# Kernel tuning notes

Hardware: AMD Instinct MI355X
Metric: run time of the kernel (lower is better)

## Reference

```python
import jax, jax.numpy as jnp
import numpy as np

B, C, H, W = 4, 128, 64, 64
CQK = C // 8


def setup_inputs() -> dict:
    key = jax.random.key(0)
    ks = jax.random.split(key, 8)
    s = 0.02
    return {
        "x": jax.random.normal(ks[0], (B, C, H, W), dtype=jnp.float32),
        "Wq": jax.random.normal(ks[1], (CQK, C), dtype=jnp.float32) * s,
        "bq": jnp.zeros((CQK,), dtype=jnp.float32),
        "Wk": jax.random.normal(ks[2], (CQK, C), dtype=jnp.float32) * s,
        "bk": jnp.zeros((CQK,), dtype=jnp.float32),
        "Wv": jax.random.normal(ks[3], (C, C), dtype=jnp.float32) * s,
        "bv": jnp.zeros((C,), dtype=jnp.float32),
        "gamma": jnp.zeros((1,), dtype=jnp.float32),
    }


def reference(x, Wq, bq, Wk, bk, Wv, bv, gamma):
    b, c, h, w = x.shape
    xf = x.reshape(b, c, h * w)                      # [b, c, n]
    # 1x1 convs == per-position channel matmuls
    q = jnp.einsum('dc,bcn->bdn', Wq, xf) + bq[None, :, None]   # [b, c/8, n]
    k = jnp.einsum('dc,bcn->bdn', Wk, xf) + bk[None, :, None]   # [b, c/8, n]
    v = jnp.einsum('ec,bcn->ben', Wv, xf) + bv[None, :, None]   # [b, c, n]
    energy = jnp.einsum('bdi,bdj->bij', q, k)        # [b, n, n]
    attn = jax.nn.softmax(energy, axis=-1)           # softmax over keys j
    out = jnp.einsum('bcj,bij->bci', v, attn)        # [b, c, n]
    out = out.reshape(b, c, h, w)
    return gamma[0] * out + x
```

## Files before the change

kernel.cpp:

```cpp
#include <hip/hip_runtime.h>
#include <hip/hip_bf16.h>


#define BN 4
#define CC 128
#define NN 4096
#define DQK 16
#define KVB 64

typedef float f32x16 __attribute__((ext_vector_type(16)));
typedef short s16x8 __attribute__((ext_vector_type(8)));
typedef unsigned short u16;

union FragU { unsigned u[4]; s16x8 v; };

__device__ inline u16 to_bf16(float f) {
  __hip_bfloat16 h = __float2bfloat16(f);
  return *reinterpret_cast<u16*>(&h);
}
__device__ inline unsigned pack_bf16(float lo, float hi) {
  return ((unsigned)to_bf16(hi) << 16) | (unsigned)to_bf16(lo);
}
__device__ inline float bf16lo_f(unsigned u) {
  return __builtin_bit_cast(float, u << 16);
}
__device__ inline float bf16hi_f(unsigned u) {
  return __builtin_bit_cast(float, u & 0xffff0000u);
}

__global__ __launch_bounds__(320) void proj_kernel(
    const float* __restrict__ x,
    const float* __restrict__ Wq, const float* __restrict__ bq,
    const float* __restrict__ Wk, const float* __restrict__ bk,
    const float* __restrict__ Wv, const float* __restrict__ bv,
    u16* __restrict__ Qt, u16* __restrict__ Kt, u16* __restrict__ Vb)
{
  __shared__ float xs[CC * 32];
  const int tid = threadIdx.x;
  const int wave = tid >> 6;
  const int lane = tid & 63;
  const int l31 = lane & 31, h = lane >> 5;
  const int bid = blockIdx.x;
  const int b = bid >> 7;
  const int n0 = (bid & 127) * 32;

  const float* xb = x + ((size_t)b * CC) * NN + n0;
  #pragma unroll
  for (int k = 0; k < 4; ++k) {
    int idx4 = tid + 320 * k;
    if (idx4 < 1024) {
      int c = idx4 >> 3;
      int nn4 = (idx4 & 7) * 4;
      float4 vv = *reinterpret_cast<const float4*>(xb + (size_t)c * NN + nn4);
      *reinterpret_cast<float4*>(&xs[c * 32 + nn4]) = vv;
    }
  }
  __syncthreads();

  s16x8 bx[8];
  #pragma unroll
  for (int ks = 0; ks < 8; ++ks) {
    FragU f;
    #pragma unroll
    for (int q = 0; q < 4; ++q) {
      int c = 16 * ks + 8 * h + 2 * q;
      f.u[q] = pack_bf16(xs[c * 32 + l31], xs[(c + 1) * 32 + l31]);
    }
    bx[ks] = f.v;
  }

  f32x16 acc;
  #pragma unroll
  for (int r = 0; r < 16; ++r) acc[r] = 0.f;

  const float LOG2E = 1.44269504088896340736f;

  if (wave == 0) {
    const float* wrow = (l31 < 16) ? (Wq + (size_t)l31 * CC)
                                   : (Wk + (size_t)(l31 - 16) * CC);
    #pragma unroll
    for (int ks = 0; ks < 8; ++ks) {
      const float* wp = wrow + 16 * ks + 8 * h;
      float4 w0 = *reinterpret_cast<const float4*>(wp);
      float4 w1 = *reinterpret_cast<const float4*>(wp + 4);
      FragU a;
      a.u[0] = pack_bf16(w0.x, w0.y); a.u[1] = pack_bf16(w0.z, w0.w);
      a.u[2] = pack_bf16(w1.x, w1.y); a.u[3] = pack_bf16(w1.z, w1.w);
      acc = __builtin_amdgcn_mfma_f32_32x32x16_bf16(a.v, bx[ks], acc, 0, 0, 0);
    }
    #pragma unroll
    for (int r = 0; r < 16; ++r) {
      int row = (r & 3) + 8 * (r >> 2) + 4 * h;
      float val = acc[r];
      if (row < 16) {
        val = (val + bq[row]) * LOG2E;
        Qt[((size_t)b * NN + n0 + l31) * DQK + row] = to_bf16(val);
      } else {
        val += bk[row - 16];
        Kt[((size_t)b * NN + n0 + l31) * DQK + (row - 16)] = to_bf16(val);
      }
    }
  } else {
    const int rt = wave - 1;
    const float* vrow = Wv + (size_t)(rt * 32 + l31) * CC;
    #pragma unroll
    for (int ks = 0; ks < 8; ++ks) {
      const float* wp = vrow + 16 * ks + 8 * h;
      float4 w0 = *reinterpret_cast<const float4*>(wp);
      float4 w1 = *reinterpret_cast<const float4*>(wp + 4);
      FragU a;
      a.u[0] = pack_bf16(w0.x, w0.y); a.u[1] = pack_bf16(w0.z, w0.w);
      a.u[2] = pack_bf16(w1.x, w1.y); a.u[3] = pack_bf16(w1.z, w1.w);
      acc = __builtin_amdgcn_mfma_f32_32x32x16_bf16(a.v, bx[ks], acc, 0, 0, 0);
    }
    #pragma unroll
    for (int r = 0; r < 16; ++r) {
      int e = rt * 32 + (r & 3) + 8 * (r >> 2) + 4 * h;
      Vb[((size_t)b * CC + e) * NN + n0 + l31] = to_bf16(acc[r] + bv[e]);
    }
  }
}

__global__ __launch_bounds__(512, 4) void flash_kernel(
    const u16* __restrict__ Qt, const u16* __restrict__ Kt,
    const u16* __restrict__ Vb,
    u16* __restrict__ Opart, float* __restrict__ mstat,
    float* __restrict__ lstat, int JS)
{
  __shared__ u16 Vs[2][CC * KVB];
  const int tid = threadIdx.x;
  const int wv = tid >> 6;
  const int lane = tid & 63;
  const int l31 = lane & 31, h = lane >> 5;
  const int qb = blockIdx.x & 15;
  const int bs = blockIdx.x >> 4;
  const int b = bs / JS, sg = bs % JS;
  const int i0 = qb * 256 + wv * 32;
  const int seglen = NN / JS;
  const int j_begin = sg * seglen;
  const int niter = seglen / KVB;

  const int sc0 = tid >> 3;
  const int so = (tid & 7) * 16;
  const int sw0 = (sc0 & 7) << 4;

  const u16* Kb = Kt + (size_t)b * NN * DQK;
  const u16* Vbb = Vb + (size_t)b * CC * NN;

  s16x8 qf = *reinterpret_cast<const s16x8*>(
      Qt + ((size_t)b * NN + i0 + l31) * DQK + 8 * h);

  f32x16 zero;
  #pragma unroll
  for (int r = 0; r < 16; ++r) zero[r] = 0.f;
  f32x16 acc[4];
  #pragma unroll
  for (int ct = 0; ct < 4; ++ct) acc[ct] = zero;
  float m_run = -__builtin_inff();
  float l_run = 0.f;

  {
    s16x8 g0 = *reinterpret_cast<const s16x8*>(
        Vbb + (size_t)sc0 * NN + j_begin + so / 2);
    s16x8 g1 = *reinterpret_cast<const s16x8*>(
        Vbb + (size_t)(64 + sc0) * NN + j_begin + so / 2);
    *reinterpret_cast<s16x8*>(&Vs[0][sc0 * KVB + ((so ^ sw0) >> 1)]) = g0;
    *reinterpret_cast<s16x8*>(&Vs[0][(64 + sc0) * KVB + ((so ^ sw0) >> 1)]) = g1;
  }
  s16x8 kf0 = *reinterpret_cast<const s16x8*>(
      Kb + (size_t)(j_begin + l31) * DQK + 8 * h);
  s16x8 kf1 = *reinterpret_cast<const s16x8*>(
      Kb + (size_t)(j_begin + 32 + l31) * DQK + 8 * h);
  __syncthreads();

  const int rsw = (l31 & 7) << 4;

  for (int t = 0; t < niter; ++t) {
    const int cur = t & 1;
    s16x8 g0, g1, nk0, nk1;
    const bool more = (t + 1 < niter);
    if (more) {
      const int jn = j_begin + (t + 1) * KVB;
      g0 = *reinterpret_cast<const s16x8*>(
          Vbb + (size_t)sc0 * NN + jn + so / 2);
      g1 = *reinterpret_cast<const s16x8*>(
          Vbb + (size_t)(64 + sc0) * NN + jn + so / 2);
      nk0 = *reinterpret_cast<const s16x8*>(
          Kb + (size_t)(jn + l31) * DQK + 8 * h);
      nk1 = *reinterpret_cast<const s16x8*>(
          Kb + (size_t)(jn + 32 + l31) * DQK + 8 * h);
    }

    #pragma unroll
    for (int s = 0; s < 2; ++s) {
      f32x16 sv = __builtin_amdgcn_mfma_f32_32x32x16_bf16(
          s ? kf1 : kf0, qf, zero, 0, 0, 0);

      float mx01 = fmaxf(sv[0], sv[1]),  mx23 = fmaxf(sv[2], sv[3]);
      float mx45 = fmaxf(sv[4], sv[5]),  mx67 = fmaxf(sv[6], sv[7]);
      float mx89 = fmaxf(sv[8], sv[9]),  mxab = fmaxf(sv[10], sv[11]);
      float mxcd = fmaxf(sv[12], sv[13]), mxef = fmaxf(sv[14], sv[15]);
      float tmax = fmaxf(fmaxf(fmaxf(mx01, mx23), fmaxf(mx45, mx67)),
                         fmaxf(fmaxf(mx89, mxab), fmaxf(mxcd, mxef)));
      float cmb = fmaxf(tmax, __shfl_xor(tmax, 32));
      float m_new = (cmb > m_run + 8.f) ? cmb : m_run;
      if (__any(m_new > m_run)) {
        float alpha = __builtin_amdgcn_exp2f(m_run - m_new);
        l_run *= alpha;
        #pragma unroll
        for (int ct = 0; ct < 4; ++ct)
          #pragma unroll
          for (int r = 0; r < 16; ++r) acc[ct][r] *= alpha;
        m_run = m_new;
      }

      float p[16];
      #pragma unroll
      for (int r = 0; r < 16; ++r)
        p[r] = __builtin_amdgcn_exp2f(sv[r] - m_run);
      float s01 = p[0] + p[1],  s23 = p[2] + p[3];
      float s45 = p[4] + p[5],  s67 = p[6] + p[7];
      float s89 = p[8] + p[9],  sab = p[10] + p[11];
      float scd = p[12] + p[13], sef = p[14] + p[15];
      l_run += ((s01 + s23) + (s45 + s67)) + ((s89 + sab) + (scd + sef));

      unsigned w[8], xw[8];
      #pragma unroll
      for (int q = 0; q < 8; ++q) w[q] = pack_bf16(p[2 * q], p[2 * q + 1]);
      #pragma unroll
      for (int q = 0; q < 8; ++q)
        xw[q] = (unsigned)__shfl_xor((int)w[q], 32);
      FragU f0, f1;
      f0.u[0] = h ? xw[2] : w[0];
      f0.u[1] = h ? xw[3] : w[1];
      f0.u[2] = h ? w[2] : xw[0];
      f0.u[3] = h ? w[3] : xw[1];
      f1.u[0] = h ? xw[6] : w[4];
      f1.u[1] = h ? xw[7] : w[5];
      f1.u[2] = h ? w[6] : xw[4];
      f1.u[3] = h ? w[7] : xw[5];

      #pragma unroll
      for (int ct = 0; ct < 4; ++ct) {
        const int c = 32 * ct + l31;
        s16x8 va = *reinterpret_cast<const s16x8*>(
            &Vs[cur][c * KVB + (((s * 64 + h * 16) ^ rsw) >> 1)]);
        s16x8 vb2 = *reinterpret_cast<const s16x8*>(
            &Vs[cur][c * KVB + (((s * 64 + 32 + h * 16) ^ rsw) >> 1)]);
        acc[ct] = __builtin_amdgcn_mfma_f32_32x32x16_bf16(va, f0.v,
                                                          acc[ct], 0, 0, 0);
        acc[ct] = __builtin_amdgcn_mfma_f32_32x32x16_bf16(vb2, f1.v,
                                                          acc[ct], 0, 0, 0);
      }
    }

    if (more) {
      *reinterpret_cast<s16x8*>(
          &Vs[cur ^ 1][sc0 * KVB + ((so ^ sw0) >> 1)]) = g0;
      *reinterpret_cast<s16x8*>(
          &Vs[cur ^ 1][(64 + sc0) * KVB + ((so ^ sw0) >> 1)]) = g1;
      kf0 = nk0; kf1 = nk1;
    }
    __syncthreads();
  }

  float l_tot = l_run + __shfl_xor(l_run, 32);

  u16* Ob = Opart + ((size_t)(b * JS + sg) * CC) * NN;
  #pragma unroll
  for (int ct = 0; ct < 4; ++ct)
    #pragma unroll
    for (int r = 0; r < 16; ++r) {
      int c = 32 * ct + (r & 3) + 8 * (r >> 2) + 4 * h;
      Ob[(size_t)c * NN + i0 + l31] = to_bf16(acc[ct][r]);
    }
  if (lane < 32) {
    mstat[((size_t)(b * JS + sg)) * NN + i0 + l31] = m_run;
    lstat[((size_t)(b * JS + sg)) * NN + i0 + l31] = l_tot;
  }
}

template <int JS>
__global__ __launch_bounds__(256) void merge_kernel(
    const u16* __restrict__ Opart, const float* __restrict__ mstat,
    const float* __restrict__ lstat, const float* __restrict__ x,
    const float* __restrict__ gamma, float* __restrict__ out)
{
  const int tid = threadIdx.x;
  const int il = tid & 63;
  const int cg = tid >> 6;
  const int bid = blockIdx.x;
  const int b = bid >> 8;
  const int rem = bid & 255;
  const int i = (((rem >> 3) << 6) + il) * 2;
  const int c0 = ((rem & 7) * 4 + cg) * 4;

  float m0 = -__builtin_inff(), m1 = m0;
  float ms0[JS], ms1[JS];
  #pragma unroll
  for (int s = 0; s < JS; ++s) {
    const float* mp = mstat + ((size_t)(b * JS + s)) * NN + i;
    ms0[s] = mp[0]; ms1[s] = mp[1];
    m0 = fmaxf(m0, ms0[s]); m1 = fmaxf(m1, ms1[s]);
  }
  float d0 = 0.f, d1 = 0.f;
  float w0[JS], w1[JS];
  #pragma unroll
  for (int s = 0; s < JS; ++s) {
    const float* lp = lstat + ((size_t)(b * JS + s)) * NN + i;
    w0[s] = __builtin_amdgcn_exp2f(ms0[s] - m0);
    w1[s] = __builtin_amdgcn_exp2f(ms1[s] - m1);
    d0 += w0[s] * lp[0];
    d1 += w1[s] * lp[1];
  }
  const float g = gamma[0];
  const float g0 = g / d0, g1 = g / d1;
  #pragma unroll
  for (int s = 0; s < JS; ++s) { w0[s] *= g0; w1[s] *= g1; }

  #pragma unroll
  for (int cc = 0; cc < 4; ++cc) {
    int c = c0 + cc;
    float o0 = 0.f, o1 = 0.f;
    #pragma unroll
    for (int s = 0; s < JS; ++s) {
      unsigned u = *reinterpret_cast<const unsigned*>(
          Opart + ((size_t)(b * JS + s) * CC + c) * NN + i);
      o0 += w0[s] * bf16lo_f(u);
      o1 += w1[s] * bf16hi_f(u);
    }
    size_t oidx = ((size_t)b * CC + c) * NN + i;
    float2 xv = *reinterpret_cast<const float2*>(x + oidx);
    float2 ov; ov.x = o0 + xv.x; ov.y = o1 + xv.y;
    *reinterpret_cast<float2*>(out + oidx) = ov;
  }
}

extern "C" void kernel_launch(void* const* d_in, const int* in_sizes, int n_in,
                              void* d_out, int out_size, void* d_ws,
                              size_t ws_size, hipStream_t stream)
{
  const float* x     = (const float*)d_in[0];
  const float* Wq    = (const float*)d_in[1];
  const float* bq    = (const float*)d_in[2];
  const float* Wk    = (const float*)d_in[3];
  const float* bk    = (const float*)d_in[4];
  const float* Wv    = (const float*)d_in[5];
  const float* bv    = (const float*)d_in[6];
  const float* gamma = (const float*)d_in[7];
  float* out = (float*)d_out;

  char* wsb = (char*)d_ws;
  const size_t szQ = (size_t)BN * NN * DQK * 2;
  const size_t szV = (size_t)BN * CC * NN * 2;
  const size_t base = 2 * szQ + szV;
  auto need = [&](size_t js) {
    return base + js * ((size_t)2 * BN * NN * 4 + (size_t)BN * CC * NN * 2);
  };
  int JS = 8;
  if (ws_size < need(8)) JS = 4;
  if (ws_size < need(4)) JS = 2;
  if (ws_size < need(2)) JS = 1;

  u16* Qt = (u16*)(wsb);
  u16* Kt = (u16*)(wsb + szQ);
  u16* Vb = (u16*)(wsb + 2 * szQ);
  float* mstat = (float*)(wsb + base);
  float* lstat = (float*)(wsb + base + (size_t)JS * BN * NN * 4);
  u16* Opart = (u16*)(wsb + base + (size_t)2 * JS * BN * NN * 4);

  proj_kernel<<<dim3(BN * 128), dim3(320), 0, stream>>>(
      x, Wq, bq, Wk, bk, Wv, bv, Qt, Kt, Vb);
  flash_kernel<<<dim3(BN * 16 * JS), dim3(512), 0, stream>>>(
      Qt, Kt, Vb, Opart, mstat, lstat, JS);
  if (JS == 8)
    merge_kernel<8><<<dim3(BN * 256), dim3(256), 0, stream>>>(
        Opart, mstat, lstat, x, gamma, out);
  else if (JS == 4)
    merge_kernel<4><<<dim3(BN * 256), dim3(256), 0, stream>>>(
        Opart, mstat, lstat, x, gamma, out);
  else if (JS == 2)
    merge_kernel<2><<<dim3(BN * 256), dim3(256), 0, stream>>>(
        Opart, mstat, lstat, x, gamma, out);
  else
    merge_kernel<1><<<dim3(BN * 256), dim3(256), 0, stream>>>(
        Opart, mstat, lstat, x, gamma, out);
}
```

Baseline: 130.1 us.

## Use packed bf16 converts, permlane32 swaps, LDS-staged projection stores, paired Opart layout

After: 126.1 us. 3.1% less time.

```diff
diff --git a/kernel.cpp b/kernel.cpp
--- a/kernel.cpp
+++ b/kernel.cpp
@@ -14,12 +14,21 @@
 
 union FragU { unsigned u[4]; s16x8 v; };
 
+#if defined(__has_builtin)
+#  if __has_builtin(__builtin_amdgcn_permlane32_swap)
+#    define PLSWAP 1
+#  endif
+#endif
+
 __device__ inline u16 to_bf16(float f) {
-  __hip_bfloat16 h = __float2bfloat16(f);
-  return *reinterpret_cast<u16*>(&h);
-}
-__device__ inline unsigned pack_bf16(float lo, float hi) {
-  return ((unsigned)to_bf16(hi) << 16) | (unsigned)to_bf16(lo);
+  unsigned u = __builtin_bit_cast(unsigned, f);
+  unsigned r = u + 0x7fffu + ((u >> 16) & 1u);
+  return (u16)(r >> 16);
+}
+__device__ inline unsigned cvt_pk(float lo, float hi) {
+  unsigned r;
+  asm("v_cvt_pk_bf16_f32 %0, %1, %2" : "=v"(r) : "v"(lo), "v"(hi));
+  return r;
 }
 __device__ inline float bf16lo_f(unsigned u) {
   return __builtin_bit_cast(float, u << 16);
@@ -28,34 +37,69 @@
   return __builtin_bit_cast(float, u & 0xffff0000u);
 }
 
-__global__ __launch_bounds__(320) void proj_kernel(
+__device__ inline void half_swap(unsigned& a, unsigned& b) {
+#ifdef PLSWAP
+  auto r = __builtin_amdgcn_permlane32_swap(a, b, false, false);
+  a = r[0]; b = r[1];
+#else
+  unsigned xa = (unsigned)__shfl_xor((int)a, 32);
+  unsigned xb = (unsigned)__shfl_xor((int)b, 32);
+  bool hi = (threadIdx.x & 32) != 0;
+  unsigned na = hi ? xb : a;
+  unsigned nb = hi ? b : xa;
+  a = na; b = nb;
+#endif
+}
+__device__ inline float max_partner(float t) {
+#ifdef PLSWAP
+  unsigned u = __builtin_bit_cast(unsigned, t);
+  auto r = __builtin_amdgcn_permlane32_swap(u, u, false, false);
+  return fmaxf(__builtin_bit_cast(float, r[0]), __builtin_bit_cast(float, r[1]));
+#else
+  return fmaxf(t, __shfl_xor(t, 32));
+#endif
+}
+__device__ inline float add_partner(float t) {
+#ifdef PLSWAP
+  unsigned u = __builtin_bit_cast(unsigned, t);
+  auto r = __builtin_amdgcn_permlane32_swap(u, u, false, false);
+  return __builtin_bit_cast(float, r[0]) + __builtin_bit_cast(float, r[1]);
+#else
+  return t + __shfl_xor(t, 32);
+#endif
+}
+
+__global__ __launch_bounds__(640) void proj_kernel(
     const float* __restrict__ x,
     const float* __restrict__ Wq, const float* __restrict__ bq,
     const float* __restrict__ Wk, const float* __restrict__ bk,
     const float* __restrict__ Wv, const float* __restrict__ bv,
     u16* __restrict__ Qt, u16* __restrict__ Kt, u16* __restrict__ Vb)
 {
-  __shared__ float xs[CC * 32];
+  __shared__ float xs[CC][64];
+  __shared__ u16 vout[CC][64];
+  __shared__ u16 qkout[2][32][32];
   const int tid = threadIdx.x;
   const int wave = tid >> 6;
   const int lane = tid & 63;
   const int l31 = lane & 31, h = lane >> 5;
-  const int bid = blockIdx.x;
-  const int b = bid >> 7;
-  const int n0 = (bid & 127) * 32;
+  const int b = blockIdx.x >> 6;
+  const int n0 = (blockIdx.x & 63) << 6;
 
   const float* xb = x + ((size_t)b * CC) * NN + n0;
   #pragma unroll
   for (int k = 0; k < 4; ++k) {
-    int idx4 = tid + 320 * k;
-    if (idx4 < 1024) {
-      int c = idx4 >> 3;
-      int nn4 = (idx4 & 7) * 4;
-      float4 vv = *reinterpret_cast<const float4*>(xb + (size_t)c * NN + nn4);
-      *reinterpret_cast<float4*>(&xs[c * 32 + nn4]) = vv;
+    int id = tid + 640 * k;
+    if (id < 2048) {
+      int c = id >> 4, f = (id & 15) * 4;
+      *reinterpret_cast<float4*>(&xs[c][f]) =
+          *reinterpret_cast<const float4*>(xb + (size_t)c * NN + f);
     }
   }
   __syncthreads();
+
+  const int nh = wave & 1, at = wave >> 1;
+  const int nc = nh * 32 + l31;
 
   s16x8 bx[8];
   #pragma unroll
@@ -64,7 +108,7 @@
     #pragma unroll
     for (int q = 0; q < 4; ++q) {
       int c = 16 * ks + 8 * h + 2 * q;
-      f.u[q] = pack_bf16(xs[c * 32 + l31], xs[(c + 1) * 32 + l31]);
+      f.u[q] = cvt_pk(xs[c][nc], xs[c + 1][nc]);
     }
     bx[ks] = f.v;
   }
@@ -75,56 +119,60 @@
 
   const float LOG2E = 1.44269504088896340736f;
 
-  if (wave == 0) {
-    const float* wrow = (l31 < 16) ? (Wq + (size_t)l31 * CC)
-                                   : (Wk + (size_t)(l31 - 16) * CC);
-    #pragma unroll
-    for (int ks = 0; ks < 8; ++ks) {
-      const float* wp = wrow + 16 * ks + 8 * h;
-      float4 w0 = *reinterpret_cast<const float4*>(wp);
-      float4 w1 = *reinterpret_cast<const float4*>(wp + 4);
-      FragU a;
-      a.u[0] = pack_bf16(w0.x, w0.y); a.u[1] = pack_bf16(w0.z, w0.w);
-      a.u[2] = pack_bf16(w1.x, w1.y); a.u[3] = pack_bf16(w1.z, w1.w);
-      acc = __builtin_amdgcn_mfma_f32_32x32x16_bf16(a.v, bx[ks], acc, 0, 0, 0);
-    }
+  const float* wrow;
+  if (at == 0)
+    wrow = (l31 < 16) ? (Wq + (size_t)l31 * CC) : (Wk + (size_t)(l31 - 16) * CC);
+  else
+    wrow = Wv + (size_t)((at - 1) * 32 + l31) * CC;
+
+  #pragma unroll
+  for (int ks = 0; ks < 8; ++ks) {
+    const float* wp = wrow + 16 * ks + 8 * h;
+    float4 w0 = *reinterpret_cast<const float4*>(wp);
+    float4 w1 = *reinterpret_cast<const float4*>(wp + 4);
+    FragU a;
+    a.u[0] = cvt_pk(w0.x, w0.y); a.u[1] = cvt_pk(w0.z, w0.w);
+    a.u[2] = cvt_pk(w1.x, w1.y); a.u[3] = cvt_pk(w1.z, w1.w);
+    acc = __builtin_amdgcn_mfma_f32_32x32x16_bf16(a.v, bx[ks], acc, 0, 0, 0);
+  }
+
+  if (at == 0) {
     #pragma unroll
     for (int r = 0; r < 16; ++r) {
       int row = (r & 3) + 8 * (r >> 2) + 4 * h;
       float val = acc[r];
-      if (row < 16) {
-        val = (val + bq[row]) * LOG2E;
-        Qt[((size_t)b * NN + n0 + l31) * DQK + row] = to_bf16(val);
-      } else {
-        val += bk[row - 16];
-        Kt[((size_t)b * NN + n0 + l31) * DQK + (row - 16)] = to_bf16(val);
-      }
+      val = (row < 16) ? (val + bq[row]) * LOG2E : (val + bk[row - 16]);
+      qkout[nh][row][l31] = to_bf16(val);
     }
   } else {
-    const int rt = wave - 1;
-    const float* vrow = Wv + (size_t)(rt * 32 + l31) * CC;
-    #pragma unroll
-    for (int ks = 0; ks < 8; ++ks) {
-      const float* wp = vrow + 16 * ks + 8 * h;
-      float4 w0 = *reinterpret_cast<const float4*>(wp);
-      float4 w1 = *reinterpret_cast<const float4*>(wp + 4);
-      FragU a;
-      a.u[0] = pack_bf16(w0.x, w0.y); a.u[1] = pack_bf16(w0.z, w0.w);
-      a.u[2] = pack_bf16(w1.x, w1.y); a.u[3] = pack_bf16(w1.z, w1.w);
-      acc = __builtin_amdgcn_mfma_f32_32x32x16_bf16(a.v, bx[ks], acc, 0, 0, 0);
-    }
     #pragma unroll
     for (int r = 0; r < 16; ++r) {
-      int e = rt * 32 + (r & 3) + 8 * (r >> 2) + 4 * h;
-      Vb[((size_t)b * CC + e) * NN + n0 + l31] = to_bf16(acc[r] + bv[e]);
-    }
+      int e = (at - 1) * 32 + (r & 3) + 8 * (r >> 2) + 4 * h;
+      vout[e][nh * 32 + l31] = to_bf16(acc[r] + bv[e]);
+    }
+  }
+  __syncthreads();
+
+  for (int id = tid; id < 1024; id += 640) {
+    int isK = id >> 9, j = id & 511;
+    int ni = j >> 3, ch = j & 7;
+    int nhh = ni >> 5, n32 = ni & 31;
+    unsigned lo = qkout[nhh][isK * 16 + 2 * ch][n32];
+    unsigned hi = qkout[nhh][isK * 16 + 2 * ch + 1][n32];
+    u16* dst = (isK ? Kt : Qt) + ((size_t)b * NN + n0 + ni) * DQK + 2 * ch;
+    *reinterpret_cast<unsigned*>(dst) = lo | (hi << 16);
+  }
+  for (int id = tid; id < 1024; id += 640) {
+    int c = id >> 3, q16 = id & 7;
+    s16x8 v = *reinterpret_cast<const s16x8*>(&vout[c][q16 * 8]);
+    *reinterpret_cast<s16x8*>(Vb + ((size_t)b * CC + c) * NN + n0 + q16 * 8) = v;
   }
 }
 
 __global__ __launch_bounds__(512, 4) void flash_kernel(
     const u16* __restrict__ Qt, const u16* __restrict__ Kt,
     const u16* __restrict__ Vb,
-    u16* __restrict__ Opart, float* __restrict__ mstat,
+    unsigned* __restrict__ Opart, float* __restrict__ mstat,
     float* __restrict__ lstat, int JS)
 {
   __shared__ u16 Vs[2][CC * KVB];
@@ -196,13 +244,14 @@
       f32x16 sv = __builtin_amdgcn_mfma_f32_32x32x16_bf16(
           s ? kf1 : kf0, qf, zero, 0, 0, 0);
 
-      float mx01 = fmaxf(sv[0], sv[1]),  mx23 = fmaxf(sv[2], sv[3]);
-      float mx45 = fmaxf(sv[4], sv[5]),  mx67 = fmaxf(sv[6], sv[7]);
-      float mx89 = fmaxf(sv[8], sv[9]),  mxab = fmaxf(sv[10], sv[11]);
-      float mxcd = fmaxf(sv[12], sv[13]), mxef = fmaxf(sv[14], sv[15]);
-      float tmax = fmaxf(fmaxf(fmaxf(mx01, mx23), fmaxf(mx45, mx67)),
-                         fmaxf(fmaxf(mx89, mxab), fmaxf(mxcd, mxef)));
-      float cmb = fmaxf(tmax, __shfl_xor(tmax, 32));
+      float t0 = fmaxf(fmaxf(sv[0], sv[1]), sv[2]);
+      float t1 = fmaxf(fmaxf(sv[3], sv[4]), sv[5]);
+      float t2 = fmaxf(fmaxf(sv[6], sv[7]), sv[8]);
+      float t3 = fmaxf(fmaxf(sv[9], sv[10]), sv[11]);
+      float t4 = fmaxf(fmaxf(sv[12], sv[13]), sv[14]);
+      float u0 = fmaxf(fmaxf(t0, t1), t2);
+      float u1 = fmaxf(fmaxf(t3, t4), sv[15]);
+      float cmb = max_partner(fmaxf(u0, u1));
       float m_new = (cmb > m_run + 8.f) ? cmb : m_run;
       if (__any(m_new > m_run)) {
         float alpha = __builtin_amdgcn_exp2f(m_run - m_new);
@@ -224,21 +273,17 @@
       float scd = p[12] + p[13], sef = p[14] + p[15];
       l_run += ((s01 + s23) + (s45 + s67)) + ((s89 + sab) + (scd + sef));
 
-      unsigned w[8], xw[8];
-      #pragma unroll
-      for (int q = 0; q < 8; ++q) w[q] = pack_bf16(p[2 * q], p[2 * q + 1]);
-      #pragma unroll
-      for (int q = 0; q < 8; ++q)
-        xw[q] = (unsigned)__shfl_xor((int)w[q], 32);
+      unsigned w0_ = cvt_pk(p[0], p[1]),  w1_ = cvt_pk(p[2], p[3]);
+      unsigned w2_ = cvt_pk(p[4], p[5]),  w3_ = cvt_pk(p[6], p[7]);
+      unsigned w4_ = cvt_pk(p[8], p[9]),  w5_ = cvt_pk(p[10], p[11]);
+      unsigned w6_ = cvt_pk(p[12], p[13]), w7_ = cvt_pk(p[14], p[15]);
+      half_swap(w0_, w2_);
+      half_swap(w1_, w3_);
+      half_swap(w4_, w6_);
+      half_swap(w5_, w7_);
       FragU f0, f1;
-      f0.u[0] = h ? xw[2] : w[0];
-      f0.u[1] = h ? xw[3] : w[1];
-      f0.u[2] = h ? w[2] : xw[0];
-      f0.u[3] = h ? w[3] : xw[1];
-      f1.u[0] = h ? xw[6] : w[4];
-      f1.u[1] = h ? xw[7] : w[5];
-      f1.u[2] = h ? w[6] : xw[4];
-      f1.u[3] = h ? w[7] : xw[5];
+      f0.u[0] = w0_; f0.u[1] = w1_; f0.u[2] = w2_; f0.u[3] = w3_;
+      f1.u[0] = w4_; f1.u[1] = w5_; f1.u[2] = w6_; f1.u[3] = w7_;
 
       #pragma unroll
       for (int ct = 0; ct < 4; ++ct) {
@@ -264,15 +309,16 @@
     __syncthreads();
   }
 
-  float l_tot = l_run + __shfl_xor(l_run, 32);
-
-  u16* Ob = Opart + ((size_t)(b * JS + sg) * CC) * NN;
+  float l_tot = add_partner(l_run);
+
+  unsigned* Ob = Opart + ((size_t)(b * JS + sg) * 64) * NN;
   #pragma unroll
   for (int ct = 0; ct < 4; ++ct)
     #pragma unroll
-    for (int r = 0; r < 16; ++r) {
-      int c = 32 * ct + (r & 3) + 8 * (r >> 2) + 4 * h;
-      Ob[(size_t)c * NN + i0 + l31] = to_bf16(acc[ct][r]);
+    for (int q = 0; q < 8; ++q) {
+      unsigned pv = cvt_pk(acc[ct][2 * q], acc[ct][2 * q + 1]);
+      int c = 32 * ct + ((2 * q) & 3) + 8 * (q >> 1) + 4 * h;
+      Ob[(size_t)(c >> 1) * NN + i0 + l31] = pv;
     }
   if (lane < 32) {
     mstat[((size_t)(b * JS + sg)) * NN + i0 + l31] = m_run;
@@ -282,7 +328,7 @@
 
 template <int JS>
 __global__ __launch_bounds__(256) void merge_kernel(
-    const u16* __restrict__ Opart, const float* __restrict__ mstat,
+    const unsigned* __restrict__ Opart, const float* __restrict__ mstat,
     const float* __restrict__ lstat, const float* __restrict__ x,
     const float* __restrict__ gamma, float* __restrict__ out)
 {
@@ -293,7 +339,7 @@
   const int b = bid >> 8;
   const int rem = bid & 255;
   const int i = (((rem >> 3) << 6) + il) * 2;
-  const int c0 = ((rem & 7) * 4 + cg) * 4;
+  const int c2 = ((rem & 7) * 4 + cg) * 2;
 
   float m0 = -__builtin_inff(), m1 = m0;
   float ms0[JS], ms1[JS];
@@ -318,20 +364,22 @@
   #pragma unroll
   for (int s = 0; s < JS; ++s) { w0[s] *= g0; w1[s] *= g1; }
 
+  float o[4][2] = {{0.f, 0.f}, {0.f, 0.f}, {0.f, 0.f}, {0.f, 0.f}};
+  #pragma unroll
+  for (int s = 0; s < JS; ++s) {
+    const unsigned* Ob = Opart + ((size_t)(b * JS + s) * 64) * NN;
+    uint2 A = *reinterpret_cast<const uint2*>(&Ob[(size_t)c2 * NN + i]);
+    uint2 Bv = *reinterpret_cast<const uint2*>(&Ob[(size_t)(c2 + 1) * NN + i]);
+    o[0][0] += w0[s] * bf16lo_f(A.x);  o[1][0] += w0[s] * bf16hi_f(A.x);
+    o[0][1] += w1[s] * bf16lo_f(A.y);  o[1][1] += w1[s] * bf16hi_f(A.y);
+    o[2][0] += w0[s] * bf16lo_f(Bv.x); o[3][0] += w0[s] * bf16hi_f(Bv.x);
+    o[2][1] += w1[s] * bf16lo_f(Bv.y); o[3][1] += w1[s] * bf16hi_f(Bv.y);
+  }
   #pragma unroll
   for (int cc = 0; cc < 4; ++cc) {
-    int c = c0 + cc;
-    float o0 = 0.f, o1 = 0.f;
-    #pragma unroll
-    for (int s = 0; s < JS; ++s) {
-      unsigned u = *reinterpret_cast<const unsigned*>(
-          Opart + ((size_t)(b * JS + s) * CC + c) * NN + i);
-      o0 += w0[s] * bf16lo_f(u);
-      o1 += w1[s] * bf16hi_f(u);
-    }
-    size_t oidx = ((size_t)b * CC + c) * NN + i;
+    size_t oidx = ((size_t)b * CC + 2 * c2 + cc) * NN + i;
     float2 xv = *reinterpret_cast<const float2*>(x + oidx);
-    float2 ov; ov.x = o0 + xv.x; ov.y = o1 + xv.y;
+    float2 ov; ov.x = o[cc][0] + xv.x; ov.y = o[cc][1] + xv.y;
     *reinterpret_cast<float2*>(out + oidx) = ov;
   }
 }
@@ -355,7 +403,7 @@
   const size_t szV = (size_t)BN * CC * NN * 2;
   const size_t base = 2 * szQ + szV;
   auto need = [&](size_t js) {
-    return base + js * ((size_t)2 * BN * NN * 4 + (size_t)BN * CC * NN * 2);
+    return base + js * ((size_t)2 * BN * NN * 4 + (size_t)BN * 64 * NN * 4);
   };
   int JS = 8;
   if (ws_size < need(8)) JS = 4;
@@ -367,9 +415,9 @@
   u16* Vb = (u16*)(wsb + 2 * szQ);
   float* mstat = (float*)(wsb + base);
   float* lstat = (float*)(wsb + base + (size_t)JS * BN * NN * 4);
-  u16* Opart = (u16*)(wsb + base + (size_t)2 * JS * BN * NN * 4);
-
-  proj_kernel<<<dim3(BN * 128), dim3(320), 0, stream>>>(
+  unsigned* Opart = (unsigned*)(wsb + base + (size_t)2 * JS * BN * NN * 4);
+
+  proj_kernel<<<dim3(BN * 64), dim3(640), 0, stream>>>(
       x, Wq, bq, Wk, bk, Wv, bv, Qt, Kt, Vb);
   flash_kernel<<<dim3(BN * 16 * JS), dim3(512), 0, stream>>>(
       Qt, Kt, Vb, Opart, mstat, lstat, JS);
```
